# Kernel tuning notes

Hardware: AMD Instinct MI355X
Metric: run time of the kernel (lower is better)

Reference implementation:

```python
import jax, jax.numpy as jnp
import numpy as np
from jax import lax

CHAR_SIZE, EMBED, HID = 20000, 128, 256
B, T = 256, 512


def setup_inputs() -> dict:
    key = jax.random.key(0)
    ks = jax.random.split(key, 12)
    s = 0.02
    return {
        "inputs": jax.random.randint(ks[0], (B, T), 0, CHAR_SIZE, dtype=jnp.int32),
        "input_end": jax.random.randint(ks[1], (B,), 0, B, dtype=jnp.int32),
        "embed_table": jax.random.normal(ks[2], (CHAR_SIZE, EMBED), jnp.float32) * s,
        "Wf": jax.random.normal(ks[3], (EMBED, 4 * HID), jnp.float32) * s,
        "Uf": jax.random.normal(ks[4], (HID, 4 * HID), jnp.float32) * s,
        "bf": jnp.zeros((4 * HID,), jnp.float32),
        "Wb": jax.random.normal(ks[5], (EMBED, 4 * HID), jnp.float32) * s,
        "Ub": jax.random.normal(ks[6], (HID, 4 * HID), jnp.float32) * s,
        "bb": jnp.zeros((4 * HID,), jnp.float32),
        "cls_W": jax.random.normal(ks[7], (2 * HID, 1), jnp.float32) * s,
        "cls_b": jnp.zeros((1,), jnp.float32),
        "ent_W": jax.random.normal(ks[8], (2 * HID, 3), jnp.float32) * s,
        "ent_b": jnp.zeros((3,), jnp.float32),
    }


def _masked_lstm(x_tbe, m_tb, W, U, b, reverse):
    """Keras-style masked LSTM; returns final hidden state [B, H].
    Masked steps carry (h, c) through unchanged."""
    Bn = x_tbe.shape[1]
    H = U.shape[0]

    def step(carry, inp):
        h, c = carry
        xt, mt = inp  # xt: [B,E], mt: [B]
        z = xt @ W + h @ U + b  # [B, 4H]
        i, f, g, o = jnp.split(z, 4, axis=-1)
        c_new = jax.nn.sigmoid(f) * c + jax.nn.sigmoid(i) * jnp.tanh(g)
        h_new = jax.nn.sigmoid(o) * jnp.tanh(c_new)
        m = mt[:, None]
        return (jnp.where(m, h_new, h), jnp.where(m, c_new, c)), None

    init = (jnp.zeros((Bn, H), x_tbe.dtype), jnp.zeros((Bn, H), x_tbe.dtype))
    (h, _), _ = lax.scan(step, init, (x_tbe, m_tb), reverse=reverse)
    return h


def reference(inputs, input_end, embed_table, Wf, Uf, bf, Wb, Ub, bb,
              cls_W, cls_b, ent_W, ent_b):
    mask = inputs > 0  # [B, T]
    embed = embed_table[inputs]  # [B, T, E]
    x_tbe = jnp.swapaxes(embed, 0, 1)  # [T, B, E]
    m_tb = mask.T  # [T, B]
    h_fwd = _masked_lstm(x_tbe, m_tb, Wf, Uf, bf, reverse=False)  # [B, H]
    h_bwd = _masked_lstm(x_tbe, m_tb, Wb, Ub, bb, reverse=True)   # [B, H]
    bivalue = jnp.concatenate([h_fwd, h_bwd], axis=-1)  # [B, 2H]
    sentence_end = bivalue[input_end]  # gather along batch axis, as in the original
    classifier_logits = jax.nn.sigmoid(sentence_end @ cls_W + cls_b)  # [B, 1]
    entity_logits = jax.nn.softmax(bivalue @ ent_W + ent_b, axis=-1)  # [B, 3]
    return classifier_logits, entity_logits
```

## Files before the change

kernel.cpp:

```cpp
#include <hip/hip_runtime.h>
#include <hip/hip_bf16.h>
#include <hip/hip_cooperative_groups.h>

#define EMBED 128
#define HID   256
#define BB    256
#define TT    512
#define G4    1024

typedef __attribute__((ext_vector_type(8))) short short8;
typedef __attribute__((ext_vector_type(4))) float f32x4;

#define OFF_WUP   0
#define SZ_WUP    (2*8*4*32*384*2)
#define OFF_BP    (OFF_WUP + SZ_WUP)
#define SZ_BP     (2*8*4*32*4)
#define OFF_XHAT  (OFF_BP + SZ_BP)
#define SZ_XHAT   ((size_t)BB*TT*EMBED*2)
#define OFF_HBUF  (OFF_XHAT + SZ_XHAT)
#define SZ_HBUF   (2*2*BB*HID*2)
#define OFF_HFIN  (OFF_HBUF + SZ_HBUF)
#define SZ_HFIN   (2*BB*HID*4)
#define OFF_FLAGS (OFF_HFIN + SZ_HFIN)
#define SZ_FLAGS  (2*8*8*4*64*4)
#define OFF_XCD   (OFF_FLAGS + SZ_FLAGS)
#define SZ_XCD    (128*16*4)

#define SPIN_GUARD (1 << 14)
#define HS_GUARD   (1 << 20)

__global__ void pack_kernel(const float* __restrict__ Wf, const float* __restrict__ Uf,
                            const float* __restrict__ bf,
                            const float* __restrict__ Wb, const float* __restrict__ Ub,
                            const float* __restrict__ bb,
                            __hip_bfloat16* __restrict__ WUp, float* __restrict__ bp) {
    int flat = blockIdx.x * 256 + threadIdx.x;
    int k = flat % 384;
    int rest = flat / 384;
    int jc   = rest & 31;
    int gate = (rest >> 5) & 3;
    int jg   = (rest >> 7) & 7;
    int dir  = rest >> 10;
    int J = gate * 256 + jg * 32 + jc;
    const float* W = dir ? Wb : Wf;
    const float* U = dir ? Ub : Uf;
    float v = (k < 128) ? W[(size_t)k * G4 + J] : U[(size_t)(k - 128) * G4 + J];
    WUp[flat] = __float2bfloat16(v);
    if (k == 0) {
        const float* bias = dir ? bb : bf;
        bp[rest] = bias[J];
    }
}

__global__ void gather_kernel(const int* __restrict__ inputs, const float* __restrict__ embed,
                              __hip_bfloat16* __restrict__ xhat) {
    int row = blockIdx.x * 2 + (threadIdx.x >> 7);
    int col = threadIdx.x & 127;
    int tok = inputs[row];
    xhat[(size_t)row * EMBED + col] = __float2bfloat16(embed[(size_t)tok * EMBED + col]);
}

__global__ void preclean_kernel() {
    if (threadIdx.x == 0) {
        asm volatile("buffer_wbl2 sc1\n\t"
                     "s_waitcnt vmcnt(0)\n\t"
                     "buffer_inv sc1\n\t"
                     "s_waitcnt vmcnt(0)" ::: "memory");
    }
}

__global__ void init_flags_kernel(int* __restrict__ p) {
    int i = blockIdx.x * 256 + threadIdx.x;
    int* q = p + i;
    unsigned z = 0;
    asm volatile("global_store_dword %0, %1, off sc0 sc1" :: "v"(q), "v"(z) : "memory");
}

__device__ __forceinline__ float frcp(float x) {
    float r;
    asm("v_rcp_f32 %0, %1" : "=v"(r) : "v"(x));
    return r;
}
__device__ __forceinline__ float sigf(float x)  { return frcp(1.f + __expf(-x)); }
__device__ __forceinline__ float ftanh(float x) { return 2.f * frcp(1.f + __expf(-2.f * x)) - 1.f; }

template<bool FAST>
__device__ __forceinline__ void lstm_loop(
        int dir, int jg, int bg, int wid, int lane,
        const int* __restrict__ inputs, const short* __restrict__ xrow,
        short* __restrict__ hbufs, int* __restrict__ flags,
        const short8 (*wfrag)[12], const float* bias,
        float* c_st, float* h_st, int brow0, int mrow0, int l15, int lhi, int jch) {

    const int rh = wid >> 1;
    int* myflag = flags + ((((dir * 8 + jg) * 8 + bg) * 4) + wid) * 64;
    const int l16 = lane & 15;
    int* pollp = flags + ((((dir * 8 + (l16 >> 1)) * 8 + bg) * 4) + (2 * rh + (l16 & 1))) * 64;

    const int   dstep = dir ? -1 : 1;
    const short* xptr = xrow + (size_t)(dir ? (TT - 1) : 0) * EMBED + 8 * lhi;
    const int*  mkp   = inputs + (size_t)brow0 * TT + (dir ? (TT - 1) : 0);
    const int*  mkp2  = mkp + 2 * TT;
    const short* hrd0 = hbufs + (size_t)(dir * 2) * BB * HID
                      + (size_t)(mrow0 + l15) * HID + 8 * lhi;
    const short* hrd1 = hrd0 + BB * HID;
    short* hwr0 = hbufs + (size_t)(dir * 2) * BB * HID
                + (size_t)brow0 * HID + jg * 32 + jch * 16 + l15;
    short* hwr1 = hwr0 + BB * HID;

    short8 xf[4];
    int mk_cur[4], mk_nxt[4];
#pragma unroll
    for (int kt = 0; kt < 4; ++kt)
        xf[kt] = *(const short8*)(xptr + kt * 32);
    mk_cur[0] = mkp[0]; mk_cur[1] = mkp[TT]; mk_cur[2] = mkp2[0]; mk_cur[3] = mkp2[TT];
    xptr += dstep * EMBED; mkp += dstep; mkp2 += dstep;

    for (int s = 0; s < TT; ++s) {
        f32x4 acc[4];
#pragma unroll
        for (int g = 0; g < 4; ++g) {
            acc[g][0] = bias[g]; acc[g][1] = bias[g]; acc[g][2] = bias[g]; acc[g][3] = bias[g];
        }
#pragma unroll
        for (int kt = 0; kt < 4; ++kt)
#pragma unroll
            for (int g = 0; g < 4; ++g)
                acc[g] = __builtin_amdgcn_mfma_f32_16x16x32_bf16(xf[kt], wfrag[g][kt], acc[g], 0, 0, 0);

        if (s != 0) {
            {
                int fv, guard = 0;
                if constexpr (FAST) {
                    do {
                        asm volatile("global_load_dword %0, %1, off sc1\n\t"
                                     "s_waitcnt vmcnt(0)"
                                     : "=v"(fv) : "v"(pollp) : "memory");
                        if (++guard > SPIN_GUARD) break;
                    } while (__any(fv < s));
                } else {
                    do {
                        asm volatile("global_load_dword %0, %1, off sc0 sc1\n\t"
                                     "s_waitcnt vmcnt(0)"
                                     : "=v"(fv) : "v"(pollp) : "memory");
                        if (++guard > SPIN_GUARD) break;
                    } while (__any(fv < s));
                }
            }

            short8 hf[8];
            const short* hbase = (s & 1) ? hrd1 : hrd0;
            if constexpr (FAST) {
                asm volatile(
                    "global_load_dwordx4 %0, %8, off sc1\n\t"
                    "global_load_dwordx4 %1, %8, off offset:64 sc1\n\t"
                    "global_load_dwordx4 %2, %8, off offset:128 sc1\n\t"
                    "global_load_dwordx4 %3, %8, off offset:192 sc1\n\t"
                    "global_load_dwordx4 %4, %8, off offset:256 sc1\n\t"
                    "global_load_dwordx4 %5, %8, off offset:320 sc1\n\t"
                    "global_load_dwordx4 %6, %8, off offset:384 sc1\n\t"
                    "global_load_dwordx4 %7, %8, off offset:448 sc1\n\t"
                    "s_waitcnt vmcnt(0)"
                    : "=&v"(hf[0]), "=&v"(hf[1]), "=&v"(hf[2]), "=&v"(hf[3]),
                      "=&v"(hf[4]), "=&v"(hf[5]), "=&v"(hf[6]), "=&v"(hf[7])
                    : "v"(hbase) : "memory");
            } else {
                asm volatile(
                    "global_load_dwordx4 %0, %8, off sc0 sc1\n\t"
                    "global_load_dwordx4 %1, %8, off offset:64 sc0 sc1\n\t"
                    "global_load_dwordx4 %2, %8, off offset:128 sc0 sc1\n\t"
                    "global_load_dwordx4 %3, %8, off offset:192 sc0 sc1\n\t"
                    "global_load_dwordx4 %4, %8, off offset:256 sc0 sc1\n\t"
                    "global_load_dwordx4 %5, %8, off offset:320 sc0 sc1\n\t"
                    "global_load_dwordx4 %6, %8, off offset:384 sc0 sc1\n\t"
                    "global_load_dwordx4 %7, %8, off offset:448 sc0 sc1\n\t"
                    "s_waitcnt vmcnt(0)"
                    : "=&v"(hf[0]), "=&v"(hf[1]), "=&v"(hf[2]), "=&v"(hf[3]),
                      "=&v"(hf[4]), "=&v"(hf[5]), "=&v"(hf[6]), "=&v"(hf[7])
                    : "v"(hbase) : "memory");
            }
            __builtin_amdgcn_sched_barrier(0);

            if (s + 1 < TT) {
#pragma unroll
                for (int kt = 0; kt < 4; ++kt)
                    xf[kt] = *(const short8*)(xptr + kt * 32);
                mk_nxt[0] = mkp[0]; mk_nxt[1] = mkp[TT];
                mk_nxt[2] = mkp2[0]; mk_nxt[3] = mkp2[TT];
                xptr += dstep * EMBED; mkp += dstep; mkp2 += dstep;
            }

#pragma unroll
            for (int kt = 0; kt < 8; ++kt)
#pragma unroll
                for (int g = 0; g < 4; ++g)
                    acc[g] = __builtin_amdgcn_mfma_f32_16x16x32_bf16(hf[kt], wfrag[g][kt + 4], acc[g], 0, 0, 0);
        } else {
#pragma unroll
            for (int kt = 0; kt < 4; ++kt)
                xf[kt] = *(const short8*)(xptr + kt * 32);
            mk_nxt[0] = mkp[0]; mk_nxt[1] = mkp[TT];
            mk_nxt[2] = mkp2[0]; mk_nxt[3] = mkp2[TT];
            xptr += dstep * EMBED; mkp += dstep; mkp2 += dstep;
        }

        unsigned hv16[4];
#pragma unroll
        for (int r = 0; r < 4; ++r) {
            float zi = acc[0][r];
            float zf = acc[1][r];
            float zg = acc[2][r];
            float zo = acc[3][r];
            float cn = sigf(zf) * c_st[r] + sigf(zi) * ftanh(zg);
            float hn = sigf(zo) * ftanh(cn);
            if (mk_cur[r] > 0) { c_st[r] = cn; h_st[r] = hn; }
            __hip_bfloat16 hbf = __float2bfloat16(h_st[r]);
            hv16[r] = (unsigned)(*(unsigned short*)&hbf);
        }
#pragma unroll
        for (int r = 0; r < 4; ++r) mk_cur[r] = mk_nxt[r];

        {
            const short* sb = ((s + 1) & 1) ? hwr1 : hwr0;
            if constexpr (FAST) {
                asm volatile(
                    "global_store_short %4, %0, off sc0\n\t"
                    "global_store_short %4, %1, off offset:512 sc0\n\t"
                    "global_store_short %4, %2, off offset:1024 sc0\n\t"
                    "global_store_short %4, %3, off offset:1536 sc0\n\t"
                    "s_waitcnt vmcnt(0)"
                    :: "v"(hv16[0]), "v"(hv16[1]), "v"(hv16[2]), "v"(hv16[3]), "v"(sb)
                    : "memory");
                if (lane == 0) {
                    int val = s + 1;
                    asm volatile("global_store_dword %0, %1, off sc0"
                                 :: "v"(myflag), "v"(val) : "memory");
                }
            } else {
                asm volatile(
                    "global_store_short %4, %0, off sc0 sc1\n\t"
                    "global_store_short %4, %1, off offset:512 sc0 sc1\n\t"
                    "global_store_short %4, %2, off offset:1024 sc0 sc1\n\t"
                    "global_store_short %4, %3, off offset:1536 sc0 sc1\n\t"
                    "s_waitcnt vmcnt(0)"
                    :: "v"(hv16[0]), "v"(hv16[1]), "v"(hv16[2]), "v"(hv16[3]), "v"(sb)
                    : "memory");
                if (lane == 0) {
                    int val = s + 1;
                    asm volatile("global_store_dword %0, %1, off sc0 sc1"
                                 :: "v"(myflag), "v"(val) : "memory");
                }
            }
        }
    }
}

__launch_bounds__(256, 1)
__global__ void lstm_kernel(const int* __restrict__ inputs,
                            const __hip_bfloat16* __restrict__ xhat,
                            const __hip_bfloat16* __restrict__ WUp,
                            const float* __restrict__ bp,
                            __hip_bfloat16* __restrict__ hbuf,
                            float* __restrict__ hfinal,
                            int* __restrict__ flags,
                            int* __restrict__ xcdtab) {
    const int bid = blockIdx.x;
    const int jg  = bid >> 4;
    const int dir = (bid >> 3) & 1;
    const int bg  = bid & 7;
    const int tid = threadIdx.x;
    const int wid = tid >> 6;
    const int lane = tid & 63;
    const int l15 = lane & 15, lhi = lane >> 4;
    const int jch = wid & 1;
    const int mrow0 = bg * 32 + (wid >> 1) * 16;
    const int brow0 = mrow0 + 4 * lhi;

    short8 wfrag[4][12];
    const short* wu = (const short*)WUp + (size_t)(dir * 8 + jg) * 4 * 32 * 384;
#pragma unroll
    for (int g = 0; g < 4; ++g)
#pragma unroll
        for (int kt = 0; kt < 12; ++kt)
            wfrag[g][kt] = *(const short8*)(wu + (size_t)(g * 32 + jch * 16 + l15) * 384 + kt * 32 + 8 * lhi);

    float bias[4];
#pragma unroll
    for (int g = 0; g < 4; ++g)
        bias[g] = bp[((dir * 8 + jg) * 4 + g) * 32 + jch * 16 + l15];

    int myxcd;
    asm volatile("s_getreg_b32 %0, hwreg(HW_REG_XCC_ID)" : "=s"(myxcd));
    if (tid == 0) {
        int* mp = xcdtab + bid * 16;
        int pv = 0x100 | myxcd;
        asm volatile("global_store_dword %0, %1, off sc0 sc1" :: "v"(mp), "v"(pv) : "memory");
    }
    int fast;
    {
        const int l8 = lane & 7;
        int* pp = xcdtab + ((l8 * 16) + dir * 8 + bg) * 16;
        int e, guard = 0;
        do {
            asm volatile("global_load_dword %0, %1, off sc0 sc1\n\t"
                         "s_waitcnt vmcnt(0)"
                         : "=v"(e) : "v"(pp) : "memory");
            if (++guard > HS_GUARD) break;
        } while (__any(e == 0));
        fast = (__all(e == (0x100 | myxcd))) ? 1 : 0;
    }

    float c_st[4] = {0, 0, 0, 0};
    float h_st[4] = {0, 0, 0, 0};
    const short* xrow = (const short*)xhat + (size_t)(mrow0 + l15) * TT * EMBED;
    short* hbufs = (short*)hbuf;

    if (fast)
        lstm_loop<true>(dir, jg, bg, wid, lane, inputs, xrow, hbufs, flags,
                        wfrag, bias, c_st, h_st, brow0, mrow0, l15, lhi, jch);
    else
        lstm_loop<false>(dir, jg, bg, wid, lane, inputs, xrow, hbufs, flags,
                         wfrag, bias, c_st, h_st, brow0, mrow0, l15, lhi, jch);

#pragma unroll
    for (int r = 0; r < 4; ++r)
        hfinal[((size_t)dir * BB + brow0 + r) * HID + jg * 32 + jch * 16 + l15] = h_st[r];
}

__global__ void epilogue_kernel(const int* __restrict__ input_end,
                                const float* __restrict__ hfinal,
                                const float* __restrict__ cls_W, const float* __restrict__ cls_b,
                                const float* __restrict__ ent_W, const float* __restrict__ ent_b,
                                float* __restrict__ out) {
    int b = blockIdx.x;
    int lane = threadIdx.x;
    int ie = input_end[b];
    float pe0 = 0, pe1 = 0, pe2 = 0, pc = 0;
    for (int k = lane; k < 2 * HID; k += 64) {
        float bv, se;
        if (k < HID) {
            bv = hfinal[(size_t)b * HID + k];
            se = hfinal[(size_t)ie * HID + k];
        } else {
            bv = hfinal[(size_t)(BB + b) * HID + (k - HID)];
            se = hfinal[(size_t)(BB + ie) * HID + (k - HID)];
        }
        pe0 += bv * ent_W[k * 3 + 0];
        pe1 += bv * ent_W[k * 3 + 1];
        pe2 += bv * ent_W[k * 3 + 2];
        pc  += se * cls_W[k];
    }
    for (int off = 32; off; off >>= 1) {
        pe0 += __shfl_down(pe0, off);
        pe1 += __shfl_down(pe1, off);
        pe2 += __shfl_down(pe2, off);
        pc  += __shfl_down(pc, off);
    }
    if (lane == 0) {
        float l0 = pe0 + ent_b[0], l1 = pe1 + ent_b[1], l2 = pe2 + ent_b[2];
        float m = fmaxf(l0, fmaxf(l1, l2));
        float e0 = __expf(l0 - m), e1 = __expf(l1 - m), e2 = __expf(l2 - m);
        float ssum = e0 + e1 + e2;
        out[256 + b * 3 + 0] = e0 / ssum;
        out[256 + b * 3 + 1] = e1 / ssum;
        out[256 + b * 3 + 2] = e2 / ssum;
        float cl = pc + cls_b[0];
        out[b] = 1.f / (1.f + __expf(-cl));
    }
}

extern "C" void kernel_launch(void* const* d_in, const int* in_sizes, int n_in,
                              void* d_out, int out_size, void* d_ws, size_t ws_size,
                              hipStream_t stream) {
    const int*   inputs    = (const int*)d_in[0];
    const int*   input_end = (const int*)d_in[1];
    const float* embed     = (const float*)d_in[2];
    const float* Wf        = (const float*)d_in[3];
    const float* Uf        = (const float*)d_in[4];
    const float* bf        = (const float*)d_in[5];
    const float* Wb        = (const float*)d_in[6];
    const float* Ub        = (const float*)d_in[7];
    const float* bb        = (const float*)d_in[8];
    const float* cls_W     = (const float*)d_in[9];
    const float* cls_b     = (const float*)d_in[10];
    const float* ent_W     = (const float*)d_in[11];
    const float* ent_b     = (const float*)d_in[12];
    float* out = (float*)d_out;

    char* ws = (char*)d_ws;
    __hip_bfloat16* WUp    = (__hip_bfloat16*)(ws + OFF_WUP);
    float*          bp     = (float*)(ws + OFF_BP);
    __hip_bfloat16* xhat   = (__hip_bfloat16*)(ws + OFF_XHAT);
    __hip_bfloat16* hbuf   = (__hip_bfloat16*)(ws + OFF_HBUF);
    float*          hfinal = (float*)(ws + OFF_HFIN);
    int*            flags  = (int*)(ws + OFF_FLAGS);
    int*            xcdtab = (int*)(ws + OFF_XCD);

    preclean_kernel<<<64, 64, 0, stream>>>();
    init_flags_kernel<<<136, 256, 0, stream>>>(flags);
    pack_kernel<<<3072, 256, 0, stream>>>(Wf, Uf, bf, Wb, Ub, bb, WUp, bp);
    gather_kernel<<<BB * TT / 2, 256, 0, stream>>>(inputs, embed, xhat);

    void* args[] = {(void*)&inputs, (void*)&xhat, (void*)&WUp, (void*)&bp,
                    (void*)&hbuf, (void*)&hfinal, (void*)&flags, (void*)&xcdtab};
    hipLaunchCooperativeKernel((void*)lstm_kernel, dim3(128), dim3(256), args, 0, stream);

    epilogue_kernel<<<BB, 64, 0, stream>>>(input_end, hfinal, cls_W, cls_b, ent_W, ent_b, out);
}
```

Before: 995.0 us.

## Replace per-wave flags with step-tagged hidden-state words for inter-block sync

Each bf16 hidden value is now stored in a 32-bit word whose upper half holds the step tag. Readers poll a sentinel word, then reload the whole h tile until every tag matches, so the separate flag store, flag poll and store-side waitcnt are gone. This cuts one global round trip per step from the recurrent critical path. In exchange, hidden-state traffic doubles and the loaded words must be repacked with perm instructions before the MFMA.

```diff
diff --git a/kernel.cpp b/kernel.cpp
--- a/kernel.cpp
+++ b/kernel.cpp
@@ -10,6 +10,7 @@
 
 typedef __attribute__((ext_vector_type(8))) short short8;
 typedef __attribute__((ext_vector_type(4))) float f32x4;
+typedef __attribute__((ext_vector_type(4))) unsigned u32x4;
 
 #define OFF_WUP   0
 #define SZ_WUP    (2*8*4*32*384*2)
@@ -18,12 +19,10 @@
 #define OFF_XHAT  (OFF_BP + SZ_BP)
 #define SZ_XHAT   ((size_t)BB*TT*EMBED*2)
 #define OFF_HBUF  (OFF_XHAT + SZ_XHAT)
-#define SZ_HBUF   (2*2*BB*HID*2)
+#define SZ_HBUF   (2*2*BB*HID*4)
 #define OFF_HFIN  (OFF_HBUF + SZ_HBUF)
 #define SZ_HFIN   (2*BB*HID*4)
-#define OFF_FLAGS (OFF_HFIN + SZ_HFIN)
-#define SZ_FLAGS  (2*8*8*4*64*4)
-#define OFF_XCD   (OFF_FLAGS + SZ_FLAGS)
+#define OFF_XCD   (OFF_HFIN + SZ_HFIN)
 #define SZ_XCD    (128*16*4)
 
 #define SPIN_GUARD (1 << 14)
@@ -69,7 +68,7 @@
     }
 }
 
-__global__ void init_flags_kernel(int* __restrict__ p) {
+__global__ void init_xcd_kernel(int* __restrict__ p) {
     int i = blockIdx.x * 256 + threadIdx.x;
     int* q = p + i;
     unsigned z = 0;
@@ -88,25 +87,23 @@
 __device__ __forceinline__ void lstm_loop(
         int dir, int jg, int bg, int wid, int lane,
         const int* __restrict__ inputs, const short* __restrict__ xrow,
-        short* __restrict__ hbufs, int* __restrict__ flags,
+        unsigned* __restrict__ hbufu,
         const short8 (*wfrag)[12], const float* bias,
         float* c_st, float* h_st, int brow0, int mrow0, int l15, int lhi, int jch) {
-
-    const int rh = wid >> 1;
-    int* myflag = flags + ((((dir * 8 + jg) * 8 + bg) * 4) + wid) * 64;
-    const int l16 = lane & 15;
-    int* pollp = flags + ((((dir * 8 + (l16 >> 1)) * 8 + bg) * 4) + (2 * rh + (l16 & 1))) * 64;
 
     const int   dstep = dir ? -1 : 1;
     const short* xptr = xrow + (size_t)(dir ? (TT - 1) : 0) * EMBED + 8 * lhi;
     const int*  mkp   = inputs + (size_t)brow0 * TT + (dir ? (TT - 1) : 0);
     const int*  mkp2  = mkp + 2 * TT;
-    const short* hrd0 = hbufs + (size_t)(dir * 2) * BB * HID
-                      + (size_t)(mrow0 + l15) * HID + 8 * lhi;
-    const short* hrd1 = hrd0 + BB * HID;
-    short* hwr0 = hbufs + (size_t)(dir * 2) * BB * HID
-                + (size_t)brow0 * HID + jg * 32 + jch * 16 + l15;
-    short* hwr1 = hwr0 + BB * HID;
+    const unsigned* hrd0 = hbufu + (size_t)(dir * 2) * BB * HID
+                         + (size_t)(mrow0 + l15) * HID + 8 * lhi;
+    const unsigned* hrd1 = hrd0 + BB * HID;
+    const unsigned* sen0 = hbufu + (size_t)(dir * 2) * BB * HID
+                         + (size_t)(mrow0 + 3) * HID + (lane & 15) * 16;
+    const unsigned* sen1 = sen0 + BB * HID;
+    unsigned* hwr0 = hbufu + (size_t)(dir * 2) * BB * HID
+                   + (size_t)brow0 * HID + jg * 32 + jch * 16 + l15;
+    unsigned* hwr1 = hwr0 + BB * HID;
 
     short8 xf[4];
     int mk_cur[4], mk_nxt[4];
@@ -129,55 +126,92 @@
                 acc[g] = __builtin_amdgcn_mfma_f32_16x16x32_bf16(xf[kt], wfrag[g][kt], acc[g], 0, 0, 0);
 
         if (s != 0) {
+            const unsigned want = (unsigned)s << 16;
+
             {
-                int fv, guard = 0;
-                if constexpr (FAST) {
-                    do {
+                const unsigned* sp = (s & 1) ? sen1 : sen0;
+                unsigned sv; int guard = 0;
+                for (;;) {
+                    if constexpr (FAST)
                         asm volatile("global_load_dword %0, %1, off sc1\n\t"
                                      "s_waitcnt vmcnt(0)"
-                                     : "=v"(fv) : "v"(pollp) : "memory");
-                        if (++guard > SPIN_GUARD) break;
-                    } while (__any(fv < s));
-                } else {
-                    do {
+                                     : "=&v"(sv) : "v"(sp) : "memory");
+                    else
                         asm volatile("global_load_dword %0, %1, off sc0 sc1\n\t"
                                      "s_waitcnt vmcnt(0)"
-                                     : "=v"(fv) : "v"(pollp) : "memory");
-                        if (++guard > SPIN_GUARD) break;
-                    } while (__any(fv < s));
+                                     : "=&v"(sv) : "v"(sp) : "memory");
+                    if (!__any(((sv ^ want) & 0xffff0000u) != 0)) break;
+                    if (++guard > SPIN_GUARD) break;
                 }
             }
 
-            short8 hf[8];
-            const short* hbase = (s & 1) ? hrd1 : hrd0;
-            if constexpr (FAST) {
-                asm volatile(
-                    "global_load_dwordx4 %0, %8, off sc1\n\t"
-                    "global_load_dwordx4 %1, %8, off offset:64 sc1\n\t"
-                    "global_load_dwordx4 %2, %8, off offset:128 sc1\n\t"
-                    "global_load_dwordx4 %3, %8, off offset:192 sc1\n\t"
-                    "global_load_dwordx4 %4, %8, off offset:256 sc1\n\t"
-                    "global_load_dwordx4 %5, %8, off offset:320 sc1\n\t"
-                    "global_load_dwordx4 %6, %8, off offset:384 sc1\n\t"
-                    "global_load_dwordx4 %7, %8, off offset:448 sc1\n\t"
-                    "s_waitcnt vmcnt(0)"
-                    : "=&v"(hf[0]), "=&v"(hf[1]), "=&v"(hf[2]), "=&v"(hf[3]),
-                      "=&v"(hf[4]), "=&v"(hf[5]), "=&v"(hf[6]), "=&v"(hf[7])
-                    : "v"(hbase) : "memory");
-            } else {
-                asm volatile(
-                    "global_load_dwordx4 %0, %8, off sc0 sc1\n\t"
-                    "global_load_dwordx4 %1, %8, off offset:64 sc0 sc1\n\t"
-                    "global_load_dwordx4 %2, %8, off offset:128 sc0 sc1\n\t"
-                    "global_load_dwordx4 %3, %8, off offset:192 sc0 sc1\n\t"
-                    "global_load_dwordx4 %4, %8, off offset:256 sc0 sc1\n\t"
-                    "global_load_dwordx4 %5, %8, off offset:320 sc0 sc1\n\t"
-                    "global_load_dwordx4 %6, %8, off offset:384 sc0 sc1\n\t"
-                    "global_load_dwordx4 %7, %8, off offset:448 sc0 sc1\n\t"
-                    "s_waitcnt vmcnt(0)"
-                    : "=&v"(hf[0]), "=&v"(hf[1]), "=&v"(hf[2]), "=&v"(hf[3]),
-                      "=&v"(hf[4]), "=&v"(hf[5]), "=&v"(hf[6]), "=&v"(hf[7])
-                    : "v"(hbase) : "memory");
+            u32x4 hv[16];
+            {
+                const unsigned* hb = (s & 1) ? hrd1 : hrd0;
+                unsigned bad; int guard = 0;
+                for (;;) {
+                    if constexpr (FAST) {
+                        asm volatile(
+                            "global_load_dwordx4 %0, %8, off sc1\n\t"
+                            "global_load_dwordx4 %1, %8, off offset:16 sc1\n\t"
+                            "global_load_dwordx4 %2, %8, off offset:128 sc1\n\t"
+                            "global_load_dwordx4 %3, %8, off offset:144 sc1\n\t"
+                            "global_load_dwordx4 %4, %8, off offset:256 sc1\n\t"
+                            "global_load_dwordx4 %5, %8, off offset:272 sc1\n\t"
+                            "global_load_dwordx4 %6, %8, off offset:384 sc1\n\t"
+                            "global_load_dwordx4 %7, %8, off offset:400 sc1"
+                            : "=&v"(hv[0]), "=&v"(hv[1]), "=&v"(hv[2]), "=&v"(hv[3]),
+                              "=&v"(hv[4]), "=&v"(hv[5]), "=&v"(hv[6]), "=&v"(hv[7])
+                            : "v"(hb) : "memory");
+                        asm volatile(
+                            "global_load_dwordx4 %0, %8, off offset:512 sc1\n\t"
+                            "global_load_dwordx4 %1, %8, off offset:528 sc1\n\t"
+                            "global_load_dwordx4 %2, %8, off offset:640 sc1\n\t"
+                            "global_load_dwordx4 %3, %8, off offset:656 sc1\n\t"
+                            "global_load_dwordx4 %4, %8, off offset:768 sc1\n\t"
+                            "global_load_dwordx4 %5, %8, off offset:784 sc1\n\t"
+                            "global_load_dwordx4 %6, %8, off offset:896 sc1\n\t"
+                            "global_load_dwordx4 %7, %8, off offset:912 sc1\n\t"
+                            "s_waitcnt vmcnt(0)"
+                            : "=&v"(hv[8]), "=&v"(hv[9]), "=&v"(hv[10]), "=&v"(hv[11]),
+                              "=&v"(hv[12]), "=&v"(hv[13]), "=&v"(hv[14]), "=&v"(hv[15])
+                            : "v"(hb) : "memory");
+                    } else {
+                        asm volatile(
+                            "global_load_dwordx4 %0, %8, off sc0 sc1\n\t"
+                            "global_load_dwordx4 %1, %8, off offset:16 sc0 sc1\n\t"
+                            "global_load_dwordx4 %2, %8, off offset:128 sc0 sc1\n\t"
+                            "global_load_dwordx4 %3, %8, off offset:144 sc0 sc1\n\t"
+                            "global_load_dwordx4 %4, %8, off offset:256 sc0 sc1\n\t"
+                            "global_load_dwordx4 %5, %8, off offset:272 sc0 sc1\n\t"
+                            "global_load_dwordx4 %6, %8, off offset:384 sc0 sc1\n\t"
+                            "global_load_dwordx4 %7, %8, off offset:400 sc0 sc1"
+                            : "=&v"(hv[0]), "=&v"(hv[1]), "=&v"(hv[2]), "=&v"(hv[3]),
+                              "=&v"(hv[4]), "=&v"(hv[5]), "=&v"(hv[6]), "=&v"(hv[7])
+                            : "v"(hb) : "memory");
+                        asm volatile(
+                            "global_load_dwordx4 %0, %8, off offset:512 sc0 sc1\n\t"
+                            "global_load_dwordx4 %1, %8, off offset:528 sc0 sc1\n\t"
+                            "global_load_dwordx4 %2, %8, off offset:640 sc0 sc1\n\t"
+                            "global_load_dwordx4 %3, %8, off offset:656 sc0 sc1\n\t"
+                            "global_load_dwordx4 %4, %8, off offset:768 sc0 sc1\n\t"
+                            "global_load_dwordx4 %5, %8, off offset:784 sc0 sc1\n\t"
+                            "global_load_dwordx4 %6, %8, off offset:896 sc0 sc1\n\t"
+                            "global_load_dwordx4 %7, %8, off offset:912 sc0 sc1\n\t"
+                            "s_waitcnt vmcnt(0)"
+                            : "=&v"(hv[8]), "=&v"(hv[9]), "=&v"(hv[10]), "=&v"(hv[11]),
+                              "=&v"(hv[12]), "=&v"(hv[13]), "=&v"(hv[14]), "=&v"(hv[15])
+                            : "v"(hb) : "memory");
+                    }
+                    bad = 0;
+#pragma unroll
+                    for (int i = 0; i < 16; ++i)
+#pragma unroll
+                        for (int j = 0; j < 4; ++j)
+                            bad |= (hv[i][j] ^ want) & 0xffff0000u;
+                    if (!__any(bad != 0)) break;
+                    if (++guard > SPIN_GUARD) break;
+                }
             }
             __builtin_amdgcn_sched_barrier(0);
 
@@ -191,10 +225,16 @@
             }
 
 #pragma unroll
-            for (int kt = 0; kt < 8; ++kt)
+            for (int kt = 0; kt < 8; ++kt) {
+                union { unsigned u[4]; short8 s8; } pk;
+                pk.u[0] = __builtin_amdgcn_perm(hv[2*kt][1],   hv[2*kt][0],   0x05040100u);
+                pk.u[1] = __builtin_amdgcn_perm(hv[2*kt][3],   hv[2*kt][2],   0x05040100u);
+                pk.u[2] = __builtin_amdgcn_perm(hv[2*kt+1][1], hv[2*kt+1][0], 0x05040100u);
+                pk.u[3] = __builtin_amdgcn_perm(hv[2*kt+1][3], hv[2*kt+1][2], 0x05040100u);
 #pragma unroll
                 for (int g = 0; g < 4; ++g)
-                    acc[g] = __builtin_amdgcn_mfma_f32_16x16x32_bf16(hf[kt], wfrag[g][kt + 4], acc[g], 0, 0, 0);
+                    acc[g] = __builtin_amdgcn_mfma_f32_16x16x32_bf16(pk.s8, wfrag[g][kt + 4], acc[g], 0, 0, 0);
+            }
         } else {
 #pragma unroll
             for (int kt = 0; kt < 4; ++kt)
@@ -204,52 +244,43 @@
             xptr += dstep * EMBED; mkp += dstep; mkp2 += dstep;
         }
 
-        unsigned hv16[4];
-#pragma unroll
-        for (int r = 0; r < 4; ++r) {
-            float zi = acc[0][r];
-            float zf = acc[1][r];
-            float zg = acc[2][r];
-            float zo = acc[3][r];
-            float cn = sigf(zf) * c_st[r] + sigf(zi) * ftanh(zg);
-            float hn = sigf(zo) * ftanh(cn);
-            if (mk_cur[r] > 0) { c_st[r] = cn; h_st[r] = hn; }
-            __hip_bfloat16 hbf = __float2bfloat16(h_st[r]);
-            hv16[r] = (unsigned)(*(unsigned short*)&hbf);
+        unsigned tv[4];
+        {
+            const unsigned tagp = (unsigned)(s + 1) << 16;
+#pragma unroll
+            for (int r = 0; r < 4; ++r) {
+                float zi = acc[0][r];
+                float zf = acc[1][r];
+                float zg = acc[2][r];
+                float zo = acc[3][r];
+                float cn = sigf(zf) * c_st[r] + sigf(zi) * ftanh(zg);
+                float hn = sigf(zo) * ftanh(cn);
+                if (mk_cur[r] > 0) { c_st[r] = cn; h_st[r] = hn; }
+                __hip_bfloat16 hbf = __float2bfloat16(h_st[r]);
+                tv[r] = tagp | (unsigned)(*(unsigned short*)&hbf);
+            }
         }
 #pragma unroll
         for (int r = 0; r < 4; ++r) mk_cur[r] = mk_nxt[r];
 
-        {
-            const short* sb = ((s + 1) & 1) ? hwr1 : hwr0;
+        if (s + 1 < TT) {
+            unsigned* sb = ((s + 1) & 1) ? hwr1 : hwr0;
             if constexpr (FAST) {
                 asm volatile(
-                    "global_store_short %4, %0, off sc0\n\t"
-                    "global_store_short %4, %1, off offset:512 sc0\n\t"
-                    "global_store_short %4, %2, off offset:1024 sc0\n\t"
-                    "global_store_short %4, %3, off offset:1536 sc0\n\t"
-                    "s_waitcnt vmcnt(0)"
-                    :: "v"(hv16[0]), "v"(hv16[1]), "v"(hv16[2]), "v"(hv16[3]), "v"(sb)
+                    "global_store_dword %4, %0, off sc0\n\t"
+                    "global_store_dword %4, %1, off offset:1024 sc0\n\t"
+                    "global_store_dword %4, %2, off offset:2048 sc0\n\t"
+                    "global_store_dword %4, %3, off offset:3072 sc0"
+                    :: "v"(tv[0]), "v"(tv[1]), "v"(tv[2]), "v"(tv[3]), "v"(sb)
                     : "memory");
-                if (lane == 0) {
-                    int val = s + 1;
-                    asm volatile("global_store_dword %0, %1, off sc0"
-                                 :: "v"(myflag), "v"(val) : "memory");
-                }
             } else {
                 asm volatile(
-                    "global_store_short %4, %0, off sc0 sc1\n\t"
-                    "global_store_short %4, %1, off offset:512 sc0 sc1\n\t"
-                    "global_store_short %4, %2, off offset:1024 sc0 sc1\n\t"
-                    "global_store_short %4, %3, off offset:1536 sc0 sc1\n\t"
-                    "s_waitcnt vmcnt(0)"
-                    :: "v"(hv16[0]), "v"(hv16[1]), "v"(hv16[2]), "v"(hv16[3]), "v"(sb)
+                    "global_store_dword %4, %0, off sc0 sc1\n\t"
+                    "global_store_dword %4, %1, off offset:1024 sc0 sc1\n\t"
+                    "global_store_dword %4, %2, off offset:2048 sc0 sc1\n\t"
+                    "global_store_dword %4, %3, off offset:3072 sc0 sc1"
+                    :: "v"(tv[0]), "v"(tv[1]), "v"(tv[2]), "v"(tv[3]), "v"(sb)
                     : "memory");
-                if (lane == 0) {
-                    int val = s + 1;
-                    asm volatile("global_store_dword %0, %1, off sc0 sc1"
-                                 :: "v"(myflag), "v"(val) : "memory");
-                }
             }
         }
     }
@@ -260,9 +291,8 @@
                             const __hip_bfloat16* __restrict__ xhat,
                             const __hip_bfloat16* __restrict__ WUp,
                             const float* __restrict__ bp,
-                            __hip_bfloat16* __restrict__ hbuf,
+                            unsigned* __restrict__ hbufu,
                             float* __restrict__ hfinal,
-                            int* __restrict__ flags,
                             int* __restrict__ xcdtab) {
     const int bid = blockIdx.x;
     const int jg  = bid >> 4;
@@ -313,13 +343,12 @@
     float c_st[4] = {0, 0, 0, 0};
     float h_st[4] = {0, 0, 0, 0};
     const short* xrow = (const short*)xhat + (size_t)(mrow0 + l15) * TT * EMBED;
-    short* hbufs = (short*)hbuf;
 
     if (fast)
-        lstm_loop<true>(dir, jg, bg, wid, lane, inputs, xrow, hbufs, flags,
+        lstm_loop<true>(dir, jg, bg, wid, lane, inputs, xrow, hbufu,
                         wfrag, bias, c_st, h_st, brow0, mrow0, l15, lhi, jch);
     else
-        lstm_loop<false>(dir, jg, bg, wid, lane, inputs, xrow, hbufs, flags,
+        lstm_loop<false>(dir, jg, bg, wid, lane, inputs, xrow, hbufu,
                          wfrag, bias, c_st, h_st, brow0, mrow0, l15, lhi, jch);
 
 #pragma unroll
@@ -391,18 +420,17 @@
     __hip_bfloat16* WUp    = (__hip_bfloat16*)(ws + OFF_WUP);
     float*          bp     = (float*)(ws + OFF_BP);
     __hip_bfloat16* xhat   = (__hip_bfloat16*)(ws + OFF_XHAT);
-    __hip_bfloat16* hbuf   = (__hip_bfloat16*)(ws + OFF_HBUF);
+    unsigned*       hbufu  = (unsigned*)(ws + OFF_HBUF);
     float*          hfinal = (float*)(ws + OFF_HFIN);
-    int*            flags  = (int*)(ws + OFF_FLAGS);
     int*            xcdtab = (int*)(ws + OFF_XCD);
 
     preclean_kernel<<<64, 64, 0, stream>>>();
-    init_flags_kernel<<<136, 256, 0, stream>>>(flags);
+    init_xcd_kernel<<<8, 256, 0, stream>>>(xcdtab);
     pack_kernel<<<3072, 256, 0, stream>>>(Wf, Uf, bf, Wb, Ub, bb, WUp, bp);
     gather_kernel<<<BB * TT / 2, 256, 0, stream>>>(inputs, embed, xhat);
 
     void* args[] = {(void*)&inputs, (void*)&xhat, (void*)&WUp, (void*)&bp,
-                    (void*)&hbuf, (void*)&hfinal, (void*)&flags, (void*)&xcdtab};
+                    (void*)&hbufu, (void*)&hfinal, (void*)&xcdtab};
     hipLaunchCooperativeKernel((void*)lstm_kernel, dim3(128), dim3(256), args, 0, stream);
 
     epilogue_kernel<<<BB, 64, 0, stream>>>(input_end, hfinal, cls_W, cls_b, ent_W, ent_b, out);
```

After: 1.642 ms. 65.1% more time.

## Pack per-wave step flags into shared cache lines and interleave h stores with gate math

Applied to the files above, without the earlier changes.

Replaces the padded one-flag-per-cache-line layout with a compact layout where the 16 producer flags a consumer wave polls sit in one 32-int line, so each poll lane reads adjacent slots. The h stores are now issued inside the gate-activation loop instead of after it, so store latency overlaps the remaining math before a single waitcnt. This is meant to reduce cross-block synchronisation latency per timestep. The risk is contention from many producers writing the same line, and possibly an incorrect polling mapping or init size.

```diff
diff --git a/kernel.cpp b/kernel.cpp
--- a/kernel.cpp
+++ b/kernel.cpp
@@ -22,7 +22,7 @@
 #define OFF_HFIN  (OFF_HBUF + SZ_HBUF)
 #define SZ_HFIN   (2*BB*HID*4)
 #define OFF_FLAGS (OFF_HFIN + SZ_HFIN)
-#define SZ_FLAGS  (2*8*8*4*64*4)
+#define SZ_FLAGS  (2*8*2*32*4)
 #define OFF_XCD   (OFF_FLAGS + SZ_FLAGS)
 #define SZ_XCD    (128*16*4)
 
@@ -93,9 +93,9 @@
         float* c_st, float* h_st, int brow0, int mrow0, int l15, int lhi, int jch) {
 
     const int rh = wid >> 1;
-    int* myflag = flags + ((((dir * 8 + jg) * 8 + bg) * 4) + wid) * 64;
-    const int l16 = lane & 15;
-    int* pollp = flags + ((((dir * 8 + (l16 >> 1)) * 8 + bg) * 4) + (2 * rh + (l16 & 1))) * 64;
+    int* fline  = flags + (((dir * 8 + bg) * 2) + rh) * 32;
+    int* myslot = fline + (jg * 2 + jch);
+    const int* pollp = fline + (lane & 15);
 
     const int   dstep = dir ? -1 : 1;
     const short* xptr = xrow + (size_t)(dir ? (TT - 1) : 0) * EMBED + 8 * lhi;
@@ -204,53 +204,40 @@
             xptr += dstep * EMBED; mkp += dstep; mkp2 += dstep;
         }
 
-        unsigned hv16[4];
-#pragma unroll
-        for (int r = 0; r < 4; ++r) {
-            float zi = acc[0][r];
-            float zf = acc[1][r];
-            float zg = acc[2][r];
-            float zo = acc[3][r];
-            float cn = sigf(zf) * c_st[r] + sigf(zi) * ftanh(zg);
-            float hn = sigf(zo) * ftanh(cn);
-            if (mk_cur[r] > 0) { c_st[r] = cn; h_st[r] = hn; }
-            __hip_bfloat16 hbf = __float2bfloat16(h_st[r]);
-            hv16[r] = (unsigned)(*(unsigned short*)&hbf);
-        }
-#pragma unroll
-        for (int r = 0; r < 4; ++r) mk_cur[r] = mk_nxt[r];
-
         {
             const short* sb = ((s + 1) & 1) ? hwr1 : hwr0;
-            if constexpr (FAST) {
-                asm volatile(
-                    "global_store_short %4, %0, off sc0\n\t"
-                    "global_store_short %4, %1, off offset:512 sc0\n\t"
-                    "global_store_short %4, %2, off offset:1024 sc0\n\t"
-                    "global_store_short %4, %3, off offset:1536 sc0\n\t"
-                    "s_waitcnt vmcnt(0)"
-                    :: "v"(hv16[0]), "v"(hv16[1]), "v"(hv16[2]), "v"(hv16[3]), "v"(sb)
-                    : "memory");
-                if (lane == 0) {
-                    int val = s + 1;
-                    asm volatile("global_store_dword %0, %1, off sc0"
-                                 :: "v"(myflag), "v"(val) : "memory");
-                }
-            } else {
-                asm volatile(
-                    "global_store_short %4, %0, off sc0 sc1\n\t"
-                    "global_store_short %4, %1, off offset:512 sc0 sc1\n\t"
-                    "global_store_short %4, %2, off offset:1024 sc0 sc1\n\t"
-                    "global_store_short %4, %3, off offset:1536 sc0 sc1\n\t"
-                    "s_waitcnt vmcnt(0)"
-                    :: "v"(hv16[0]), "v"(hv16[1]), "v"(hv16[2]), "v"(hv16[3]), "v"(sb)
-                    : "memory");
-                if (lane == 0) {
-                    int val = s + 1;
-                    asm volatile("global_store_dword %0, %1, off sc0 sc1"
-                                 :: "v"(myflag), "v"(val) : "memory");
-                }
+#pragma unroll
+            for (int r = 0; r < 4; ++r) {
+                float zi = acc[0][r];
+                float zf = acc[1][r];
+                float zg = acc[2][r];
+                float zo = acc[3][r];
+                float cn = sigf(zf) * c_st[r] + sigf(zi) * ftanh(zg);
+                float hn = sigf(zo) * ftanh(cn);
+                if (mk_cur[r] > 0) { c_st[r] = cn; h_st[r] = hn; }
+                __hip_bfloat16 hbf = __float2bfloat16(h_st[r]);
+                unsigned hv = (unsigned)(*(unsigned short*)&hbf);
+                const short* sp = sb + r * HID;
+                if constexpr (FAST)
+                    asm volatile("global_store_short %0, %1, off sc0"
+                                 :: "v"(sp), "v"(hv) : "memory");
+                else
+                    asm volatile("global_store_short %0, %1, off sc0 sc1"
+                                 :: "v"(sp), "v"(hv) : "memory");
             }
+        }
+#pragma unroll
+        for (int r = 0; r < 4; ++r) mk_cur[r] = mk_nxt[r];
+
+        asm volatile("s_waitcnt vmcnt(0)" ::: "memory");
+        if ((lane & 63) == 0) {
+            int val = s + 1;
+            if constexpr (FAST)
+                asm volatile("global_store_dword %0, %1, off sc0"
+                             :: "v"(myslot), "v"(val) : "memory");
+            else
+                asm volatile("global_store_dword %0, %1, off sc0 sc1"
+                             :: "v"(myslot), "v"(val) : "memory");
         }
     }
 }
@@ -397,7 +384,7 @@
     int*            xcdtab = (int*)(ws + OFF_XCD);
 
     preclean_kernel<<<64, 64, 0, stream>>>();
-    init_flags_kernel<<<136, 256, 0, stream>>>(flags);
+    init_flags_kernel<<<12, 256, 0, stream>>>(flags);
     pack_kernel<<<3072, 256, 0, stream>>>(Wf, Uf, bf, Wb, Ub, bb, WUp, bp);
     gather_kernel<<<BB * TT / 2, 256, 0, stream>>>(inputs, embed, xhat);
 
```

Result: slower. 1.150 ms (+15.6%).
